# Optimization experiments

Hardware: AMD Instinct MI355X
Metric: run time of the kernel (lower is better)

Reference implementation:

```python
import jax, jax.numpy as jnp
import numpy as np


def setup_inputs() -> dict:
    key = jax.random.key(0)
    k1, k2, k3, k4 = jax.random.split(key, 4)
    N, F, E = 131072, 512, 256
    x = jax.random.normal(k1, (N, F), dtype=jnp.float32)
    W = jax.random.normal(k2, (E, F), dtype=jnp.float32) * 0.05  # stacked weak-classifier weights
    b = jax.random.normal(k3, (E,), dtype=jnp.float32) * 0.05
    alphas = jax.random.normal(k4, (E,), dtype=jnp.float32)
    return {"x": x, "W": W, "b": b, "alphas": alphas}


def reference(x, W, b, alphas):
    # Fused version of the per-estimator Python loop:
    # per estimator e: pred_e = round(sigmoid(x @ W[e] + b[e])) in {0,1}
    logits = jnp.einsum('nf,ef->ne', x, W) + b              # [N, E]
    preds = jnp.round(jax.nn.sigmoid(logits))               # [N, E], half-to-even like torch.round
    # original casts each (alpha * pred) term to long (trunc toward zero) before accumulating
    terms = jnp.trunc(alphas[None, :] * preds)              # [N, E]
    acc = jnp.sum(terms, axis=1)                            # [N]
    return jnp.sign(acc)
```

## Files before the change

### kernel.cpp

```cpp
#include <hip/hip_runtime.h>
#include <math.h>


#define F_DIM  512
#define BM     128
#define BK     32
#define NTMAX  8
#define WSLOTS 256
#define TAU    1e-3f

typedef float f32x4  __attribute__((ext_vector_type(4)));
typedef short bf16x8 __attribute__((ext_vector_type(8)));
typedef unsigned short u16x4 __attribute__((ext_vector_type(4)));

__device__ inline unsigned short bf16_rne(float v) {
    unsigned u = __float_as_uint(v);
    u += 0x7FFFu + ((u >> 16) & 1u);
    return (unsigned short)(u >> 16);
}
__device__ inline float bf16_to_f32(unsigned short h) {
    return __uint_as_float(((unsigned)h) << 16);
}

__device__ inline void cvt8(const f32x4 a, const f32x4 b, bf16x8& hi, bf16x8& lo) {
    #pragma unroll
    for (int j = 0; j < 4; ++j) {
        const float v0 = a[j], v1 = b[j];
        const unsigned short h0 = bf16_rne(v0);
        const unsigned short h1 = bf16_rne(v1);
        hi[j]     = (short)h0;
        hi[j + 4] = (short)h1;
        lo[j]     = (short)bf16_rne(v0 - bf16_to_f32(h0));
        lo[j + 4] = (short)bf16_rne(v1 - bf16_to_f32(h1));
    }
}

__device__ __attribute__((noinline)) bool exact_pred(const float* __restrict__ xr,
                                                     const float* __restrict__ wr,
                                                     float bv) {
    double s0 = 0.0, s1 = 0.0, s2 = 0.0, s3 = 0.0;
    for (int k = 0; k < F_DIM; k += 4) {
        s0 = fma((double)xr[k + 0], (double)wr[k + 0], s0);
        s1 = fma((double)xr[k + 1], (double)wr[k + 1], s1);
        s2 = fma((double)xr[k + 2], (double)wr[k + 2], s2);
        s3 = fma((double)xr[k + 3], (double)wr[k + 3], s3);
    }
    double s = ((s0 + s1) + (s2 + s3)) + (double)bv;
    return s > 0.0;
}

__global__ __launch_bounds__(256)
void ada_prep(const float* __restrict__ W, const float* __restrict__ alphas,
              unsigned short* __restrict__ whi, unsigned short* __restrict__ wlo) {
    __shared__ int se[WSLOTS];
    __shared__ int wcnt[4];
    const int tid = threadIdx.x;

    se[tid] = 0;
    __syncthreads();
    const float t = truncf(alphas[tid]);
    const bool flag = (t != 0.0f);
    const unsigned long long m64 = __ballot(flag);
    const int lane = tid & 63, wvi = tid >> 6;
    if (lane == 0) wcnt[wvi] = __popcll(m64);
    __syncthreads();
    int off = 0;
    #pragma unroll
    for (int w = 0; w < 4; ++w) if (w < wvi) off += wcnt[w];
    if (flag) se[off + __popcll(m64 & ((1ull << lane) - 1ull))] = tid;
    __syncthreads();

    const int gstride = gridDim.x * blockDim.x;
    for (int job = blockIdx.x * blockDim.x + tid; job < WSLOTS * (F_DIM / 4); job += gstride) {
        const int col = job >> 7;
        const int k4  = (job & 127) << 2;
        const f32x4 v = *(const f32x4*)(W + (size_t)se[col] * F_DIM + k4);
        u16x4 hv, lv;
        #pragma unroll
        for (int j = 0; j < 4; ++j) {
            const unsigned short h = bf16_rne(v[j]);
            hv[j] = h;
            lv[j] = bf16_rne(v[j] - bf16_to_f32(h));
        }
        *(u16x4*)(whi + (size_t)col * F_DIM + k4) = hv;
        *(u16x4*)(wlo + (size_t)col * F_DIM + k4) = lv;
    }
}

__global__ __launch_bounds__(256, 3)
void ada_mfma2(const float* __restrict__ x, const float* __restrict__ W,
               const float* __restrict__ bias, const float* __restrict__ alphas,
               const unsigned short* __restrict__ whi, const unsigned short* __restrict__ wlo,
               float* __restrict__ out) {
    __shared__ int   se[WSLOTS];
    __shared__ float st[WSLOTS];
    __shared__ float sb[WSLOTS];
    __shared__ int   wcnt[4];

    const int tid = threadIdx.x;
    const int n0  = blockIdx.x * BM;

    se[tid] = 0; st[tid] = 0.0f; sb[tid] = 0.0f;
    __syncthreads();
    const float t = truncf(alphas[tid]);
    const bool flag = (t != 0.0f);
    const unsigned long long m64 = __ballot(flag);
    const int lane = tid & 63, wvi = tid >> 6;
    if (lane == 0) wcnt[wvi] = __popcll(m64);
    __syncthreads();
    int off = 0;
    #pragma unroll
    for (int w = 0; w < 4; ++w) if (w < wvi) off += wcnt[w];
    const int M = wcnt[0] + wcnt[1] + wcnt[2] + wcnt[3];
    if (flag) {
        const int slot = off + __popcll(m64 & ((1ull << lane) - 1ull));
        se[slot] = tid; st[slot] = t; sb[slot] = bias[tid];
    }
    __syncthreads();

    const int quad = (tid >> 4) & 3;
    const int l15  = tid & 15;
    const int rw   = (tid >> 6) * 32;

    const float* xp0 = x + (size_t)(n0 + rw + l15) * F_DIM + quad * 8;
    const float* xp1 = xp0 + (size_t)16 * F_DIM;

    int part[2][4];
    #pragma unroll
    for (int mt = 0; mt < 2; ++mt)
        #pragma unroll
        for (int r = 0; r < 4; ++r) part[mt][r] = 0;

    for (int cb = 0; cb < M; cb += 128) {
        const int Mrem = M - cb;
        const int NT   = (Mrem + 15) >> 4 < NTMAX ? (Mrem + 15) >> 4 : NTMAX;

        const unsigned short* wph = whi + (size_t)(cb + l15) * F_DIM + quad * 8;
        const unsigned short* wpl = wlo + (size_t)(cb + l15) * F_DIM + quad * 8;

        f32x4 acc[2][NTMAX];
        #pragma unroll
        for (int mt = 0; mt < 2; ++mt)
            #pragma unroll
            for (int nt = 0; nt < NTMAX; ++nt)
                acc[mt][nt] = (f32x4){0.0f, 0.0f, 0.0f, 0.0f};

        f32x4 xv0 = *(const f32x4*)(xp0);
        f32x4 xv1 = *(const f32x4*)(xp0 + 4);
        f32x4 xv2 = *(const f32x4*)(xp1);
        f32x4 xv3 = *(const f32x4*)(xp1 + 4);

        for (int k0 = 0; k0 < F_DIM; k0 += BK) {
            bf16x8 ah[2], al[2];
            cvt8(xv0, xv1, ah[0], al[0]);
            cvt8(xv2, xv3, ah[1], al[1]);

            const int kn = k0 + BK;
            if (kn < F_DIM) {
                xv0 = *(const f32x4*)(xp0 + kn);
                xv1 = *(const f32x4*)(xp0 + kn + 4);
                xv2 = *(const f32x4*)(xp1 + kn);
                xv3 = *(const f32x4*)(xp1 + kn + 4);
            }

            #pragma unroll
            for (int nt = 0; nt < NTMAX; ++nt) {
                if (nt < NT) {
                    const bf16x8 bh = *(const bf16x8*)(wph + (size_t)nt * 16 * F_DIM + k0);
                    const bf16x8 bl = *(const bf16x8*)(wpl + (size_t)nt * 16 * F_DIM + k0);
                    #pragma unroll
                    for (int mt = 0; mt < 2; ++mt) {
                        acc[mt][nt] = __builtin_amdgcn_mfma_f32_16x16x32_bf16(ah[mt], bh, acc[mt][nt], 0, 0, 0);
                        acc[mt][nt] = __builtin_amdgcn_mfma_f32_16x16x32_bf16(al[mt], bh, acc[mt][nt], 0, 0, 0);
                        acc[mt][nt] = __builtin_amdgcn_mfma_f32_16x16x32_bf16(ah[mt], bl, acc[mt][nt], 0, 0, 0);
                    }
                }
            }
        }

        #pragma unroll
        for (int nt = 0; nt < NTMAX; ++nt) {
            if (nt < NT) {
                const int col = cb + nt * 16 + l15;
                const float tv = st[col];
                if (tv != 0.0f) {
                    const float bv = sb[col];
                    const int it = (int)tv;
                    #pragma unroll
                    for (int mt = 0; mt < 2; ++mt) {
                        #pragma unroll
                        for (int r = 0; r < 4; ++r) {
                            const float logit = acc[mt][nt][r] + bv;
                            bool pred = (logit > 0.0f);
                            if (fabsf(logit) < TAU) {
                                const int row = rw + mt * 16 + quad * 4 + r;
                                pred = exact_pred(x + (size_t)(n0 + row) * F_DIM,
                                                  W + (size_t)se[col] * F_DIM, bv);
                            }
                            if (pred) part[mt][r] += it;
                        }
                    }
                }
            }
        }
    }

    #pragma unroll
    for (int mt = 0; mt < 2; ++mt) {
        #pragma unroll
        for (int r = 0; r < 4; ++r) {
            int v = part[mt][r];
            v += __shfl_xor(v, 1);
            v += __shfl_xor(v, 2);
            v += __shfl_xor(v, 4);
            v += __shfl_xor(v, 8);
            part[mt][r] = v;
        }
    }
    if (l15 == 0) {
        #pragma unroll
        for (int mt = 0; mt < 2; ++mt) {
            float4 o;
            o.x = (part[mt][0] > 0) ? 1.0f : (part[mt][0] < 0 ? -1.0f : 0.0f);
            o.y = (part[mt][1] > 0) ? 1.0f : (part[mt][1] < 0 ? -1.0f : 0.0f);
            o.z = (part[mt][2] > 0) ? 1.0f : (part[mt][2] < 0 ? -1.0f : 0.0f);
            o.w = (part[mt][3] > 0) ? 1.0f : (part[mt][3] < 0 ? -1.0f : 0.0f);
            *(float4*)(out + n0 + rw + mt * 16 + quad * 4) = o;
        }
    }
}

extern "C" void kernel_launch(void* const* d_in, const int* in_sizes, int n_in,
                              void* d_out, int out_size, void* d_ws, size_t ws_size,
                              hipStream_t stream) {
    const float* x      = (const float*)d_in[0];
    const float* W      = (const float*)d_in[1];
    const float* bias   = (const float*)d_in[2];
    const float* alphas = (const float*)d_in[3];
    float* out = (float*)d_out;

    const int n = in_sizes[0] / F_DIM;
    const int nblocks = n / BM;

    unsigned short* whi = (unsigned short*)d_ws;
    unsigned short* wlo = whi + (size_t)WSLOTS * F_DIM;

    ada_prep<<<dim3(64), dim3(256), 0, stream>>>(W, alphas, whi, wlo);
    ada_mfma2<<<dim3(nblocks), dim3(256), 0, stream>>>(x, W, bias, alphas, whi, wlo, out);
}
```

Baseline: 535.5 us.

## Pre-swizzle bf16 weight tiles and double-buffer x/W register loads

The prep kernel now writes the hi/lo bf16 weight split in a tile-major layout that matches the MFMA operand fragments, so each lane's 8-element load is contiguous across the wavefront. The main kernel drops the variable NT bound and always processes 8 column tiles, unrolling all 16 K-steps with software double-buffered register prefetch of both x and W fragments. MFMAs are interleaved across the two row tiles to hide dependency latency. This raises register pressure (launch bounds lowered to 2 blocks per CU). It also computes padded columns when M is not a multiple of 128, relying on zero-filled slots.

```diff
diff --git a/kernel.cpp b/kernel.cpp
--- a/kernel.cpp
+++ b/kernel.cpp
@@ -5,7 +5,8 @@
 #define F_DIM  512
 #define BM     128
 #define BK     32
-#define NTMAX  8
+#define KSTEPS 16
+#define NT     8
 #define WSLOTS 256
 #define TAU    1e-3f
 
@@ -70,25 +71,27 @@
     if (flag) se[off + __popcll(m64 & ((1ull << lane) - 1ull))] = tid;
     __syncthreads();
 
-    const int gstride = gridDim.x * blockDim.x;
-    for (int job = blockIdx.x * blockDim.x + tid; job < WSLOTS * (F_DIM / 4); job += gstride) {
-        const int col = job >> 7;
-        const int k4  = (job & 127) << 2;
-        const f32x4 v = *(const f32x4*)(W + (size_t)se[col] * F_DIM + k4);
-        u16x4 hv, lv;
-        #pragma unroll
-        for (int j = 0; j < 4; ++j) {
-            const unsigned short h = bf16_rne(v[j]);
-            hv[j] = h;
-            lv[j] = bf16_rne(v[j] - bf16_to_f32(h));
-        }
-        *(u16x4*)(whi + (size_t)col * F_DIM + k4) = hv;
-        *(u16x4*)(wlo + (size_t)col * F_DIM + k4) = lv;
-    }
-}
-
-__global__ __launch_bounds__(256, 3)
-void ada_mfma2(const float* __restrict__ x, const float* __restrict__ W,
+    const int job  = blockIdx.x * 256 + tid;
+    const int slot = job >> 6;
+    const int rem  = job & 63;
+    const int ks   = rem >> 2;
+    const int quad = rem & 3;
+    const int tile = slot >> 4;
+    const int l15  = slot & 15;
+
+    const float* src = W + (size_t)se[slot] * F_DIM + ks * 32 + quad * 8;
+    const f32x4 a = *(const f32x4*)(src);
+    const f32x4 b = *(const f32x4*)(src + 4);
+    bf16x8 hi, lo;
+    cvt8(a, b, hi, lo);
+
+    const size_t dst = ((size_t)(tile * 16 + ks) * 64 + (quad * 16 + l15)) * 8;
+    *(bf16x8*)(whi + dst) = hi;
+    *(bf16x8*)(wlo + dst) = lo;
+}
+
+__global__ __launch_bounds__(256, 2)
+void ada_mfma3(const float* __restrict__ x, const float* __restrict__ W,
                const float* __restrict__ bias, const float* __restrict__ alphas,
                const unsigned short* __restrict__ whi, const unsigned short* __restrict__ wlo,
                float* __restrict__ out) {
@@ -125,6 +128,9 @@
     const float* xp0 = x + (size_t)(n0 + rw + l15) * F_DIM + quad * 8;
     const float* xp1 = xp0 + (size_t)16 * F_DIM;
 
+    const unsigned short* wbh_base = whi + (size_t)lane * 8;
+    const unsigned short* wbl_base = wlo + (size_t)lane * 8;
+
     int part[2][4];
     #pragma unroll
     for (int mt = 0; mt < 2; ++mt)
@@ -132,73 +138,81 @@
         for (int r = 0; r < 4; ++r) part[mt][r] = 0;
 
     for (int cb = 0; cb < M; cb += 128) {
-        const int Mrem = M - cb;
-        const int NT   = (Mrem + 15) >> 4 < NTMAX ? (Mrem + 15) >> 4 : NTMAX;
-
-        const unsigned short* wph = whi + (size_t)(cb + l15) * F_DIM + quad * 8;
-        const unsigned short* wpl = wlo + (size_t)(cb + l15) * F_DIM + quad * 8;
-
-        f32x4 acc[2][NTMAX];
+        const int p8 = cb >> 4;
+
+        f32x4 acc[2][NT];
         #pragma unroll
         for (int mt = 0; mt < 2; ++mt)
             #pragma unroll
-            for (int nt = 0; nt < NTMAX; ++nt)
+            for (int nt = 0; nt < NT; ++nt)
                 acc[mt][nt] = (f32x4){0.0f, 0.0f, 0.0f, 0.0f};
 
-        f32x4 xv0 = *(const f32x4*)(xp0);
-        f32x4 xv1 = *(const f32x4*)(xp0 + 4);
-        f32x4 xv2 = *(const f32x4*)(xp1);
-        f32x4 xv3 = *(const f32x4*)(xp1 + 4);
-
-        for (int k0 = 0; k0 < F_DIM; k0 += BK) {
-            bf16x8 ah[2], al[2];
-            cvt8(xv0, xv1, ah[0], al[0]);
-            cvt8(xv2, xv3, ah[1], al[1]);
-
-            const int kn = k0 + BK;
-            if (kn < F_DIM) {
-                xv0 = *(const f32x4*)(xp0 + kn);
-                xv1 = *(const f32x4*)(xp0 + kn + 4);
-                xv2 = *(const f32x4*)(xp1 + kn);
-                xv3 = *(const f32x4*)(xp1 + kn + 4);
-            }
-
-            #pragma unroll
-            for (int nt = 0; nt < NTMAX; ++nt) {
-                if (nt < NT) {
-                    const bf16x8 bh = *(const bf16x8*)(wph + (size_t)nt * 16 * F_DIM + k0);
-                    const bf16x8 bl = *(const bf16x8*)(wpl + (size_t)nt * 16 * F_DIM + k0);
-                    #pragma unroll
-                    for (int mt = 0; mt < 2; ++mt) {
-                        acc[mt][nt] = __builtin_amdgcn_mfma_f32_16x16x32_bf16(ah[mt], bh, acc[mt][nt], 0, 0, 0);
-                        acc[mt][nt] = __builtin_amdgcn_mfma_f32_16x16x32_bf16(al[mt], bh, acc[mt][nt], 0, 0, 0);
-                        acc[mt][nt] = __builtin_amdgcn_mfma_f32_16x16x32_bf16(ah[mt], bl, acc[mt][nt], 0, 0, 0);
-                    }
+        f32x4  xv[2][4];
+        bf16x8 wh[2][NT], wl[2][NT];
+
+        xv[0][0] = *(const f32x4*)(xp0);
+        xv[0][1] = *(const f32x4*)(xp0 + 4);
+        xv[0][2] = *(const f32x4*)(xp1);
+        xv[0][3] = *(const f32x4*)(xp1 + 4);
+        #pragma unroll
+        for (int nt = 0; nt < NT; ++nt) {
+            const size_t o = (size_t)((p8 + nt) * 16) * 512;
+            wh[0][nt] = *(const bf16x8*)(wbh_base + o);
+            wl[0][nt] = *(const bf16x8*)(wbl_base + o);
+        }
+
+        #pragma unroll
+        for (int ks = 0; ks < KSTEPS; ++ks) {
+            const int cur = ks & 1, nxt = cur ^ 1;
+
+            if (ks + 1 < KSTEPS) {
+                const int kf = (ks + 1) * BK;
+                xv[nxt][0] = *(const f32x4*)(xp0 + kf);
+                xv[nxt][1] = *(const f32x4*)(xp0 + kf + 4);
+                xv[nxt][2] = *(const f32x4*)(xp1 + kf);
+                xv[nxt][3] = *(const f32x4*)(xp1 + kf + 4);
+                #pragma unroll
+                for (int nt = 0; nt < NT; ++nt) {
+                    const size_t o = (size_t)((p8 + nt) * 16 + ks + 1) * 512;
+                    wh[nxt][nt] = *(const bf16x8*)(wbh_base + o);
+                    wl[nxt][nt] = *(const bf16x8*)(wbl_base + o);
                 }
             }
-        }
-
-        #pragma unroll
-        for (int nt = 0; nt < NTMAX; ++nt) {
-            if (nt < NT) {
-                const int col = cb + nt * 16 + l15;
-                const float tv = st[col];
-                if (tv != 0.0f) {
-                    const float bv = sb[col];
-                    const int it = (int)tv;
+
+            bf16x8 ah0, al0, ah1, al1;
+            cvt8(xv[cur][0], xv[cur][1], ah0, al0);
+            cvt8(xv[cur][2], xv[cur][3], ah1, al1);
+
+            #pragma unroll
+            for (int nt = 0; nt < NT; ++nt) {
+                acc[0][nt] = __builtin_amdgcn_mfma_f32_16x16x32_bf16(ah0, wh[cur][nt], acc[0][nt], 0, 0, 0);
+                acc[1][nt] = __builtin_amdgcn_mfma_f32_16x16x32_bf16(ah1, wh[cur][nt], acc[1][nt], 0, 0, 0);
+                acc[0][nt] = __builtin_amdgcn_mfma_f32_16x16x32_bf16(al0, wh[cur][nt], acc[0][nt], 0, 0, 0);
+                acc[1][nt] = __builtin_amdgcn_mfma_f32_16x16x32_bf16(al1, wh[cur][nt], acc[1][nt], 0, 0, 0);
+                acc[0][nt] = __builtin_amdgcn_mfma_f32_16x16x32_bf16(ah0, wl[cur][nt], acc[0][nt], 0, 0, 0);
+                acc[1][nt] = __builtin_amdgcn_mfma_f32_16x16x32_bf16(ah1, wl[cur][nt], acc[1][nt], 0, 0, 0);
+            }
+        }
+
+        #pragma unroll
+        for (int nt = 0; nt < NT; ++nt) {
+            const int col = cb + nt * 16 + l15;
+            const float tv = st[col];
+            if (tv != 0.0f) {
+                const float bv = sb[col];
+                const int it = (int)tv;
+                #pragma unroll
+                for (int mt = 0; mt < 2; ++mt) {
                     #pragma unroll
-                    for (int mt = 0; mt < 2; ++mt) {
-                        #pragma unroll
-                        for (int r = 0; r < 4; ++r) {
-                            const float logit = acc[mt][nt][r] + bv;
-                            bool pred = (logit > 0.0f);
-                            if (fabsf(logit) < TAU) {
-                                const int row = rw + mt * 16 + quad * 4 + r;
-                                pred = exact_pred(x + (size_t)(n0 + row) * F_DIM,
-                                                  W + (size_t)se[col] * F_DIM, bv);
-                            }
-                            if (pred) part[mt][r] += it;
+                    for (int r = 0; r < 4; ++r) {
+                        const float logit = acc[mt][nt][r] + bv;
+                        bool pred = (logit > 0.0f);
+                        if (fabsf(logit) < TAU) {
+                            const int row = rw + mt * 16 + quad * 4 + r;
+                            pred = exact_pred(x + (size_t)(n0 + row) * F_DIM,
+                                              W + (size_t)se[col] * F_DIM, bv);
                         }
+                        if (pred) part[mt][r] += it;
                     }
                 }
             }
@@ -246,5 +260,5 @@
     unsigned short* wlo = whi + (size_t)WSLOTS * F_DIM;
 
     ada_prep<<<dim3(64), dim3(256), 0, stream>>>(W, alphas, whi, wlo);
-    ada_mfma2<<<dim3(nblocks), dim3(256), 0, stream>>>(x, W, bias, alphas, whi, wlo, out);
-}
+    ada_mfma3<<<dim3(nblocks), dim3(256), 0, stream>>>(x, W, bias, alphas, whi, wlo, out);
+}
```

New measurement: 622.2 us. +16.2%, slower.
